# Optimization experiments

Hardware: AMD Instinct MI355X
Metric: run time of the kernel (lower is better)

The kernel has to match this reference:

```python
import jax, jax.numpy as jnp
import numpy as np

B, T, D = 2, 2048, 1024
F_DIM = 4096
E = 8


def setup_inputs() -> dict:
    key = jax.random.key(0)
    ks = jax.random.split(key, 6)
    x = jax.random.normal(ks[0], (B, T, D), dtype=jnp.float32)
    Wr = jax.random.normal(ks[1], (E, D), dtype=jnp.float32) * 0.02  # router weight [E, D]
    W1 = jax.random.normal(ks[2], (E, F_DIM, D), dtype=jnp.float32) * 0.02  # per-expert Linear(D->F) weights
    b1 = jnp.zeros((E, F_DIM), dtype=jnp.float32)
    W2 = jax.random.normal(ks[3], (E, D, F_DIM), dtype=jnp.float32) * 0.02  # per-expert Linear(F->D) weights
    b2 = jnp.zeros((E, D), dtype=jnp.float32)
    return {"x": x, "Wr": Wr, "W1": W1, "b1": b1, "W2": W2, "b2": b2, "top_k": 2}


def reference(x, Wr, W1, b1, W2, b2, top_k):
    # router scores: [b, t, E]
    scores = jnp.einsum('btd,ed->bte', x, Wr)
    topk_vals, topk_idx = jax.lax.top_k(scores, top_k)  # [b, t, k]
    # Dense compute over all experts (E is small); grouped-GEMM equivalent of the
    # original per-token loop. hidden: [b, t, E, F]
    h = jax.nn.relu(jnp.einsum('btd,efd->btef', x, W1) + b1)
    all_out = jnp.einsum('btef,edf->bted', h, W2) + b2  # [b, t, E, D]
    # gather the top-k experts' outputs per token: [b, t, k, D]
    gathered = jnp.take_along_axis(all_out, topk_idx[..., None], axis=2)
    # FAITHFUL to source: softmax over the sequence dim (dim=-1 of [b, t]),
    # applied independently per top-k slot.
    weight = jax.nn.softmax(topk_vals, axis=1)  # [b, t, k]
    out = jnp.sum(weight[..., None] * gathered, axis=2)  # [b, t, D]
    return out
```

## Files before the change

### kernel.cpp

```cpp
#include <hip/hip_runtime.h>
#include <stdint.h>

typedef short bf16x8 __attribute__((ext_vector_type(8)));
typedef float f32x4 __attribute__((ext_vector_type(4)));

#define NTOK 4096
#define DDIM 1024
#define FDIM 4096
#define NEXP 8
#define SEQ  2048

#define FB_MAXROWS 8704
#define FB_MAXTILES 136
#define G_MAXROWS 10240
#define G_MT 40

#define GLOAD16(g, l) __builtin_amdgcn_global_load_lds( \
    (const __attribute__((address_space(1))) unsigned int*)(const void*)(g), \
    (__attribute__((address_space(3))) unsigned int*)(l), 16, 0, 0)

#define SCHEDB() __builtin_amdgcn_sched_barrier(0)

__device__ __forceinline__ unsigned short f2bf(float f) {
    union { float f; unsigned int u; } v; v.f = f;
    unsigned int u = v.u;
    unsigned int r = (u + 0x7FFFu + ((u >> 16) & 1u)) >> 16;
    return (unsigned short)r;
}
__device__ __forceinline__ unsigned int pk2(float a, float b) {
    return (unsigned int)f2bf(a) | ((unsigned int)f2bf(b) << 16);
}

__global__ __launch_bounds__(256) void cvt_kernel(
    const float* __restrict__ src, unsigned short* __restrict__ dst, int n4)
{
    int i = blockIdx.x * 256 + threadIdx.x;
    const int stride = gridDim.x * 256;
    for (; i < n4; i += stride) {
        const float4 v = ((const float4*)src)[i];
        ushort4 o;
        o.x = f2bf(v.x); o.y = f2bf(v.y); o.z = f2bf(v.z); o.w = f2bf(v.w);
        ((ushort4*)dst)[i] = o;
    }
}

__global__ __launch_bounds__(256) void router_kernel(
    const float* __restrict__ x, const float* __restrict__ Wr,
    float* __restrict__ topk_vals, int* __restrict__ topk_idx,
    int* __restrict__ counts)
{
    const int wave = threadIdx.x >> 6;
    const int lane = threadIdx.x & 63;
    const int t = blockIdx.x * 4 + wave;
    const float4* xr = (const float4*)(x + (size_t)t * DDIM);

    float acc[NEXP];
#pragma unroll
    for (int e = 0; e < NEXP; ++e) acc[e] = 0.0f;

    for (int d = lane; d < DDIM / 4; d += 64) {
        const float4 xv = xr[d];
#pragma unroll
        for (int e = 0; e < NEXP; ++e) {
            const float4 wv = ((const float4*)(Wr + e * DDIM))[d];
            acc[e] = fmaf(xv.x, wv.x, acc[e]);
            acc[e] = fmaf(xv.y, wv.y, acc[e]);
            acc[e] = fmaf(xv.z, wv.z, acc[e]);
            acc[e] = fmaf(xv.w, wv.w, acc[e]);
        }
    }
#pragma unroll
    for (int e = 0; e < NEXP; ++e) {
        for (int off = 32; off > 0; off >>= 1)
            acc[e] += __shfl_xor(acc[e], off, 64);
    }
    if (lane == 0) {
        float best = -3.4e38f, second = -3.4e38f;
        int bi = 0, si = 0;
#pragma unroll
        for (int e = 0; e < NEXP; ++e) {
            const float s = acc[e];
            if (s > best) { second = best; si = bi; best = s; bi = e; }
            else if (s > second) { second = s; si = e; }
        }
        topk_vals[t * 2 + 0] = best;
        topk_vals[t * 2 + 1] = second;
        topk_idx[t * 2 + 0] = bi;
        topk_idx[t * 2 + 1] = si;
        atomicAdd(&counts[bi], 1);
        atomicAdd(&counts[si], 1);
    }
}

__global__ __launch_bounds__(256) void softmax_seq_kernel(
    const float* __restrict__ tv, float* __restrict__ weight)
{
    const int b = blockIdx.x >> 1;
    const int k = blockIdx.x & 1;
    const float* base = tv + (size_t)b * SEQ * 2 + k;
    float* wbase = weight + (size_t)b * SEQ * 2 + k;
    __shared__ float red[256];
    const int tid = threadIdx.x;

    float m = -3.4e38f;
    for (int t = tid; t < SEQ; t += 256) m = fmaxf(m, base[t * 2]);
    red[tid] = m; __syncthreads();
    for (int s = 128; s > 0; s >>= 1) {
        if (tid < s) red[tid] = fmaxf(red[tid], red[tid + s]);
        __syncthreads();
    }
    m = red[0];
    __syncthreads();

    float sum = 0.0f;
    for (int t = tid; t < SEQ; t += 256) sum += expf(base[t * 2] - m);
    red[tid] = sum; __syncthreads();
    for (int s = 128; s > 0; s >>= 1) {
        if (tid < s) red[tid] += red[tid + s];
        __syncthreads();
    }
    const float inv = 1.0f / red[0];
    for (int t = tid; t < SEQ; t += 256)
        wbase[t * 2] = expf(base[t * 2] - m) * inv;
}

__global__ void scan_kernel(const int* __restrict__ counts,
                            int* __restrict__ padOff, int* __restrict__ cursor,
                            int padBits)
{
    if (threadIdx.x == 0) {
        const int pad = (1 << padBits) - 1;
        int o = 0;
        for (int e = 0; e < NEXP; ++e) {
            padOff[e] = o;
            o += ((counts[e] + pad) >> padBits) << padBits;
        }
        padOff[NEXP] = o;
    }
    if (threadIdx.x < NEXP) cursor[threadIdx.x] = 0;
}

__global__ __launch_bounds__(256) void scatter_kernel(
    const int* __restrict__ topk_idx, const int* __restrict__ padOff,
    int* __restrict__ cursor, int* __restrict__ perm)
{
    const int t = blockIdx.x * 256 + threadIdx.x;
#pragma unroll
    for (int k = 0; k < 2; ++k) {
        const int e = topk_idx[t * 2 + k];
        const int pos = padOff[e] + atomicAdd(&cursor[e], 1);
        perm[pos] = t * 2 + k;
    }
}


__global__ __launch_bounds__(512, 2) void gemm1_g(
    const unsigned short* __restrict__ Xb, const unsigned short* __restrict__ Wb,
    const float* __restrict__ b1, const int* __restrict__ perm,
    const int* __restrict__ padOff, unsigned short* __restrict__ h)
{
    const int bid = blockIdx.x;
    const int swz = (bid & 7) * 80 + (bid >> 3);
    const int by = swz % G_MT;
    const int bx = swz / G_MT;
    const int row0 = by * 256;
    if (row0 >= padOff[NEXP]) return;
    int e = 0;
#pragma unroll
    for (int i = 1; i < NEXP; ++i) if (row0 >= padOff[i]) e = i;

    __shared__ unsigned short As[2][256 * 64];
    __shared__ unsigned short Bs[2][256 * 64];

    const int tid = threadIdx.x;
    const int w = tid >> 6, lane = tid & 63;
    const int wr = (w >> 2) * 128;
    const int wc = (w & 3) * 64;
    const int fr = lane & 15, kg = lane >> 4;
    const int col0 = bx * 256;

    const int gchunk = ((tid & 7) ^ ((tid >> 3) & 7)) * 8;
    const int lbase = (tid >> 3) * 64 + (tid & 7) * 8;

    const unsigned short* aSrc[4];
    const unsigned short* bSrc[4];
#pragma unroll
    for (int j = 0; j < 4; ++j) {
        const int r = j * 64 + (tid >> 3);
        const int pm = perm[row0 + r];
        const int tok = (pm >= 0) ? (pm >> 1) : 0;
        aSrc[j] = Xb + (size_t)tok * DDIM + gchunk;
        bSrc[j] = Wb + ((size_t)e * FDIM + col0 + r) * DDIM + gchunk;
    }

    f32x4 acc[8][4] = {};

#define STG1(buf, koff) do { \
    _Pragma("unroll") \
    for (int j = 0; j < 4; ++j) { \
        GLOAD16(aSrc[j] + (koff), &As[buf][j * 4096 + lbase]); \
        GLOAD16(bSrc[j] + (koff), &Bs[buf][j * 4096 + lbase]); \
    } } while (0)

    const int NT = DDIM / 64;
    STG1(0, 0);
    __syncthreads();

    int cur = 0;
    for (int t = 0; t < NT; ++t) {
        if (t + 1 < NT) STG1(cur ^ 1, (t + 1) * 64);
        SCHEDB();
        const unsigned short* Ab = &As[cur][0];
        const unsigned short* Bb = &Bs[cur][0];
#pragma unroll
        for (int kk = 0; kk < 2; ++kk) {
            bf16x8 a[8], b[4];
            const int cx = (((kk << 2) | kg)) ;
#pragma unroll
            for (int m = 0; m < 8; ++m)
                a[m] = *(const bf16x8*)&Ab[(wr + m * 16 + fr) * 64 + ((cx ^ (fr & 7)) << 3)];
#pragma unroll
            for (int n = 0; n < 4; ++n)
                b[n] = *(const bf16x8*)&Bb[(wc + n * 16 + fr) * 64 + ((cx ^ (fr & 7)) << 3)];
#pragma unroll
            for (int m = 0; m < 8; ++m)
#pragma unroll
                for (int n = 0; n < 4; ++n)
                    acc[m][n] = __builtin_amdgcn_mfma_f32_16x16x32_bf16(a[m], b[n], acc[m][n], 0, 0, 0);
        }
        __syncthreads();
        cur ^= 1;
    }
#undef STG1

#pragma unroll
    for (int n = 0; n < 4; ++n) {
        const int colg = col0 + wc + n * 16 + fr;
        const float bias = b1[e * FDIM + colg];
#pragma unroll
        for (int m = 0; m < 8; ++m) {
#pragma unroll
            for (int r = 0; r < 4; ++r) {
                const int rowg = row0 + wr + m * 16 + kg * 4 + r;
                h[(size_t)rowg * FDIM + colg] = f2bf(fmaxf(acc[m][n][r] + bias, 0.0f));
            }
        }
    }
}

__global__ __launch_bounds__(512, 2) void gemm2_g(
    const unsigned short* __restrict__ h, const unsigned short* __restrict__ Wb,
    const float* __restrict__ b2, const int* __restrict__ perm,
    const int* __restrict__ padOff, const float* __restrict__ weight,
    float* __restrict__ out)
{
    const int bid = blockIdx.x;
    const int swz = (bid & 7) * 80 + (bid >> 3);
    const int by = swz % G_MT;
    const int rest = swz / G_MT;
    const int bx = rest & 3;
    const int kc = rest >> 2;
    const int row0 = by * 256;
    if (row0 >= padOff[NEXP]) return;
    int e = 0;
#pragma unroll
    for (int i = 1; i < NEXP; ++i) if (row0 >= padOff[i]) e = i;

    __shared__ unsigned short As[2][256 * 64];
    __shared__ unsigned short Bs[2][256 * 64];

    const int tid = threadIdx.x;
    const int w = tid >> 6, lane = tid & 63;
    const int wr = (w >> 2) * 128;
    const int wc = (w & 3) * 64;
    const int fr = lane & 15, kg = lane >> 4;
    const int col0 = bx * 256;
    const int kbase = kc * (FDIM / 4);

    const int gchunk = ((tid & 7) ^ ((tid >> 3) & 7)) * 8;
    const int lbase = (tid >> 3) * 64 + (tid & 7) * 8;

    const unsigned short* aSrc[4];
    const unsigned short* bSrc[4];
#pragma unroll
    for (int j = 0; j < 4; ++j) {
        const int r = j * 64 + (tid >> 3);
        aSrc[j] = h + (size_t)(row0 + r) * FDIM + kbase + gchunk;
        bSrc[j] = Wb + ((size_t)e * DDIM + col0 + r) * FDIM + kbase + gchunk;
    }

    f32x4 acc[8][4] = {};

#define STG2(buf, koff) do { \
    _Pragma("unroll") \
    for (int j = 0; j < 4; ++j) { \
        GLOAD16(aSrc[j] + (koff), &As[buf][j * 4096 + lbase]); \
        GLOAD16(bSrc[j] + (koff), &Bs[buf][j * 4096 + lbase]); \
    } } while (0)

    const int NT = (FDIM / 4) / 64;
    STG2(0, 0);
    __syncthreads();

    int cur = 0;
    for (int t = 0; t < NT; ++t) {
        if (t + 1 < NT) STG2(cur ^ 1, (t + 1) * 64);
        SCHEDB();
        const unsigned short* Ab = &As[cur][0];
        const unsigned short* Bb = &Bs[cur][0];
#pragma unroll
        for (int kk = 0; kk < 2; ++kk) {
            bf16x8 a[8], b[4];
            const int cx = (((kk << 2) | kg));
#pragma unroll
            for (int m = 0; m < 8; ++m)
                a[m] = *(const bf16x8*)&Ab[(wr + m * 16 + fr) * 64 + ((cx ^ (fr & 7)) << 3)];
#pragma unroll
            for (int n = 0; n < 4; ++n)
                b[n] = *(const bf16x8*)&Bb[(wc + n * 16 + fr) * 64 + ((cx ^ (fr & 7)) << 3)];
#pragma unroll
            for (int m = 0; m < 8; ++m)
#pragma unroll
                for (int n = 0; n < 4; ++n)
                    acc[m][n] = __builtin_amdgcn_mfma_f32_16x16x32_bf16(a[m], b[n], acc[m][n], 0, 0, 0);
        }
        __syncthreads();
        cur ^= 1;
    }
#undef STG2

#pragma unroll
    for (int n = 0; n < 4; ++n) {
        const int colg = col0 + wc + n * 16 + fr;
        const float bias = (kc == 0) ? b2[e * DDIM + colg] : 0.0f;
#pragma unroll
        for (int m = 0; m < 8; ++m) {
#pragma unroll
            for (int r = 0; r < 4; ++r) {
                const int rowg = row0 + wr + m * 16 + kg * 4 + r;
                const int pm = perm[rowg];
                if (pm >= 0) {
                    const float wgt = weight[pm];
                    atomicAdd(&out[(size_t)(pm >> 1) * DDIM + colg], (acc[m][n][r] + bias) * wgt);
                }
            }
        }
    }
}


__global__ __launch_bounds__(256) void gemm1_fb(
    const float* __restrict__ x, const float* __restrict__ W1,
    const float* __restrict__ b1, const int* __restrict__ perm,
    const int* __restrict__ padOff, unsigned short* __restrict__ h)
{
    const int row0 = blockIdx.y * 64;
    if (row0 >= padOff[NEXP]) return;
    int e = 0;
#pragma unroll
    for (int i = 1; i < NEXP; ++i) if (row0 >= padOff[i]) e = i;

    __shared__ unsigned short As[64][40];
    __shared__ unsigned short Bs[64][40];

    const int tid = threadIdx.x;
    const int srow = tid >> 2;
    const int skp = (tid & 3) << 3;

    const int pm = perm[row0 + srow];
    const float* aSrc = (pm >= 0) ? (x + (size_t)(pm >> 1) * DDIM + skp) : 0;
    const int fRow = blockIdx.x * 64 + srow;
    const float* bSrc = W1 + ((size_t)e * FDIM + fRow) * DDIM + skp;

    const int lane = tid & 63;
    const int wm = ((tid >> 7) & 1) * 32;
    const int wn = ((tid >> 6) & 1) * 32;
    const int fr = lane & 15;
    const int kg = lane >> 4;

    f32x4 acc[2][2] = {{{0,0,0,0},{0,0,0,0}},{{0,0,0,0},{0,0,0,0}}};

    for (int k0 = 0; k0 < DDIM; k0 += 32) {
        uint4 av = make_uint4(0, 0, 0, 0);
        if (aSrc) {
            const float4 lo = *(const float4*)(aSrc + k0);
            const float4 hi = *(const float4*)(aSrc + k0 + 4);
            av.x = pk2(lo.x, lo.y); av.y = pk2(lo.z, lo.w);
            av.z = pk2(hi.x, hi.y); av.w = pk2(hi.z, hi.w);
        }
        const float4 bl = *(const float4*)(bSrc + k0);
        const float4 bh = *(const float4*)(bSrc + k0 + 4);
        uint4 bv;
        bv.x = pk2(bl.x, bl.y); bv.y = pk2(bl.z, bl.w);
        bv.z = pk2(bh.x, bh.y); bv.w = pk2(bh.z, bh.w);

        __syncthreads();
        *(uint4*)&As[srow][skp] = av;
        *(uint4*)&Bs[srow][skp] = bv;
        __syncthreads();

        const bf16x8 a0 = *(const bf16x8*)&As[wm + 0  + fr][kg << 3];
        const bf16x8 a1 = *(const bf16x8*)&As[wm + 16 + fr][kg << 3];
        const bf16x8 b0 = *(const bf16x8*)&Bs[wn + 0  + fr][kg << 3];
        const bf16x8 b1v = *(const bf16x8*)&Bs[wn + 16 + fr][kg << 3];
        acc[0][0] = __builtin_amdgcn_mfma_f32_16x16x32_bf16(a0, b0,  acc[0][0], 0, 0, 0);
        acc[0][1] = __builtin_amdgcn_mfma_f32_16x16x32_bf16(a0, b1v, acc[0][1], 0, 0, 0);
        acc[1][0] = __builtin_amdgcn_mfma_f32_16x16x32_bf16(a1, b0,  acc[1][0], 0, 0, 0);
        acc[1][1] = __builtin_amdgcn_mfma_f32_16x16x32_bf16(a1, b1v, acc[1][1], 0, 0, 0);
    }

#pragma unroll
    for (int mi = 0; mi < 2; ++mi)
#pragma unroll
        for (int ni = 0; ni < 2; ++ni) {
            const int colg = blockIdx.x * 64 + wn + ni * 16 + fr;
            const float bias = b1[e * FDIM + colg];
#pragma unroll
            for (int r = 0; r < 4; ++r) {
                const int rowg = row0 + wm + mi * 16 + (kg << 2) + r;
                float v = acc[mi][ni][r] + bias;
                v = fmaxf(v, 0.0f);
                h[(size_t)rowg * FDIM + colg] = f2bf(v);
            }
        }
}

__global__ __launch_bounds__(256) void gemm2_fb(
    const unsigned short* __restrict__ h, const float* __restrict__ W2,
    const float* __restrict__ b2, const int* __restrict__ perm,
    const int* __restrict__ padOff, const float* __restrict__ weight,
    float* __restrict__ out)
{
    const int row0 = blockIdx.y * 64;
    if (row0 >= padOff[NEXP]) return;
    int e = 0;
#pragma unroll
    for (int i = 1; i < NEXP; ++i) if (row0 >= padOff[i]) e = i;

    __shared__ unsigned short As[64][40];
    __shared__ unsigned short Bs[64][40];

    const int tid = threadIdx.x;
    const int srow = tid >> 2;
    const int skp = (tid & 3) << 3;

    const unsigned short* aSrc = h + (size_t)(row0 + srow) * FDIM + skp;
    const int dRow = blockIdx.x * 64 + srow;
    const float* bSrc = W2 + ((size_t)e * DDIM + dRow) * FDIM + skp;

    const int lane = tid & 63;
    const int wm = ((tid >> 7) & 1) * 32;
    const int wn = ((tid >> 6) & 1) * 32;
    const int fr = lane & 15;
    const int kg = lane >> 4;

    f32x4 acc[2][2] = {{{0,0,0,0},{0,0,0,0}},{{0,0,0,0},{0,0,0,0}}};

    for (int k0 = 0; k0 < FDIM; k0 += 32) {
        const uint4 av = *(const uint4*)(aSrc + k0);
        const float4 bl = *(const float4*)(bSrc + k0);
        const float4 bh = *(const float4*)(bSrc + k0 + 4);
        uint4 bv;
        bv.x = pk2(bl.x, bl.y); bv.y = pk2(bl.z, bl.w);
        bv.z = pk2(bh.x, bh.y); bv.w = pk2(bh.z, bh.w);

        __syncthreads();
        *(uint4*)&As[srow][skp] = av;
        *(uint4*)&Bs[srow][skp] = bv;
        __syncthreads();

        const bf16x8 a0 = *(const bf16x8*)&As[wm + 0  + fr][kg << 3];
        const bf16x8 a1 = *(const bf16x8*)&As[wm + 16 + fr][kg << 3];
        const bf16x8 b0 = *(const bf16x8*)&Bs[wn + 0  + fr][kg << 3];
        const bf16x8 b1v = *(const bf16x8*)&Bs[wn + 16 + fr][kg << 3];
        acc[0][0] = __builtin_amdgcn_mfma_f32_16x16x32_bf16(a0, b0,  acc[0][0], 0, 0, 0);
        acc[0][1] = __builtin_amdgcn_mfma_f32_16x16x32_bf16(a0, b1v, acc[0][1], 0, 0, 0);
        acc[1][0] = __builtin_amdgcn_mfma_f32_16x16x32_bf16(a1, b0,  acc[1][0], 0, 0, 0);
        acc[1][1] = __builtin_amdgcn_mfma_f32_16x16x32_bf16(a1, b1v, acc[1][1], 0, 0, 0);
    }

#pragma unroll
    for (int mi = 0; mi < 2; ++mi)
#pragma unroll
        for (int ni = 0; ni < 2; ++ni) {
            const int colg = blockIdx.x * 64 + wn + ni * 16 + fr;
            const float bias = b2[e * DDIM + colg];
#pragma unroll
            for (int r = 0; r < 4; ++r) {
                const int rowg = row0 + wm + mi * 16 + (kg << 2) + r;
                const int pm = perm[rowg];
                if (pm >= 0) {
                    const float w = weight[pm];
                    const float v = (acc[mi][ni][r] + bias) * w;
                    atomicAdd(&out[(size_t)(pm >> 1) * DDIM + colg], v);
                }
            }
        }
}

extern "C" void kernel_launch(void* const* d_in, const int* in_sizes, int n_in,
                              void* d_out, int out_size, void* d_ws, size_t ws_size,
                              hipStream_t stream)
{
    const float* x  = (const float*)d_in[0];
    const float* Wr = (const float*)d_in[1];
    const float* W1 = (const float*)d_in[2];
    const float* b1 = (const float*)d_in[3];
    const float* W2 = (const float*)d_in[4];
    const float* b2 = (const float*)d_in[5];
    float* out = (float*)d_out;
    char* ws = (char*)d_ws;

    float* topk_vals = (float*)(ws);
    float* weight    = (float*)(ws + 32768);
    int*   topk_idx  = (int*)(ws + 65536);
    int*   counts    = (int*)(ws + 98304);
    int*   padOff    = (int*)(ws + 98368);
    int*   cursor    = (int*)(ws + 98432);
    int*   perm      = (int*)(ws + 98496);

    const size_t NEED = 151257088ULL;

    if (ws_size >= NEED) {
        unsigned short* Xb = (unsigned short*)(ws + 262144);
        unsigned short* h  = (unsigned short*)(ws + 8650752);
        unsigned short* Wb = (unsigned short*)(ws + 92536832);

        hipMemsetAsync(counts, 0, NEXP * sizeof(int), stream);
        hipMemsetAsync(perm, 0xFF, G_MAXROWS * sizeof(int), stream);
        hipMemsetAsync(out, 0, (size_t)out_size * sizeof(float), stream);

        cvt_kernel<<<2048, 256, 0, stream>>>(x, Xb, NTOK * DDIM / 4);
        cvt_kernel<<<2048, 256, 0, stream>>>(W1, Wb, NEXP * FDIM * DDIM / 4);
        router_kernel<<<NTOK / 4, 256, 0, stream>>>(x, Wr, topk_vals, topk_idx, counts);
        softmax_seq_kernel<<<4, 256, 0, stream>>>(topk_vals, weight);
        scan_kernel<<<1, 64, 0, stream>>>(counts, padOff, cursor, 8);
        scatter_kernel<<<NTOK / 256, 256, 0, stream>>>(topk_idx, padOff, cursor, perm);

        gemm1_g<<<16 * G_MT, 512, 0, stream>>>(Xb, Wb, b1, perm, padOff, h);
        cvt_kernel<<<2048, 256, 0, stream>>>(W2, Wb, NEXP * DDIM * FDIM / 4);
        gemm2_g<<<16 * G_MT, 512, 0, stream>>>(h, Wb, b2, perm, padOff, weight, out);
    } else {
        unsigned short* h = (unsigned short*)(ws + 135168);

        hipMemsetAsync(counts, 0, NEXP * sizeof(int), stream);
        hipMemsetAsync(perm, 0xFF, FB_MAXROWS * sizeof(int), stream);
        hipMemsetAsync(out, 0, (size_t)out_size * sizeof(float), stream);

        router_kernel<<<NTOK / 4, 256, 0, stream>>>(x, Wr, topk_vals, topk_idx, counts);
        softmax_seq_kernel<<<4, 256, 0, stream>>>(topk_vals, weight);
        scan_kernel<<<1, 64, 0, stream>>>(counts, padOff, cursor, 6);
        scatter_kernel<<<NTOK / 256, 256, 0, stream>>>(topk_idx, padOff, cursor, perm);

        gemm1_fb<<<dim3(FDIM / 64, FB_MAXTILES), 256, 0, stream>>>(x, W1, b1, perm, padOff, h);
        gemm2_fb<<<dim3(DDIM / 64, FB_MAXTILES), 256, 0, stream>>>(h, W2, b2, perm, padOff, weight, out);
    }
}
```

Baseline: 609.0 us.

## Use BK=32 two-stage-ahead LDS pipeline with manual waitcnt and halve GEMM2 split-K

Measured after the change: 612.9 us. No clear change (+0.6%).

```diff
diff --git a/kernel.cpp b/kernel.cpp
--- a/kernel.cpp
+++ b/kernel.cpp
@@ -19,7 +19,11 @@
     (const __attribute__((address_space(1))) unsigned int*)(const void*)(g), \
     (__attribute__((address_space(3))) unsigned int*)(l), 16, 0, 0)
 
-#define SCHEDB() __builtin_amdgcn_sched_barrier(0)
+#define WAIT_LGKM0() asm volatile("s_waitcnt lgkmcnt(0)" ::: "memory")
+#define WAIT_VM4()   asm volatile("s_waitcnt vmcnt(4)" ::: "memory")
+#define WAIT_VM0()   asm volatile("s_waitcnt vmcnt(0)" ::: "memory")
+#define SBAR()       __builtin_amdgcn_s_barrier()
+#define SCHEDB()     __builtin_amdgcn_sched_barrier(0)
 
 __device__ __forceinline__ unsigned short f2bf(float f) {
     union { float f; unsigned int u; } v; v.f = f;
@@ -169,8 +173,8 @@
 #pragma unroll
     for (int i = 1; i < NEXP; ++i) if (row0 >= padOff[i]) e = i;
 
-    __shared__ unsigned short As[2][256 * 64];
-    __shared__ unsigned short Bs[2][256 * 64];
+    __shared__ unsigned short As[2][256 * 32];
+    __shared__ unsigned short Bs[2][256 * 32];
 
     const int tid = threadIdx.x;
     const int w = tid >> 6, lane = tid & 63;
@@ -179,57 +183,53 @@
     const int fr = lane & 15, kg = lane >> 4;
     const int col0 = bx * 256;
 
-    const int gchunk = ((tid & 7) ^ ((tid >> 3) & 7)) * 8;
-    const int lbase = (tid >> 3) * 64 + (tid & 7) * 8;
-
-    const unsigned short* aSrc[4];
-    const unsigned short* bSrc[4];
-#pragma unroll
-    for (int j = 0; j < 4; ++j) {
-        const int r = j * 64 + (tid >> 3);
+    const int srow = tid >> 2;
+    const int gch = ((tid & 3) ^ (srow & 3)) * 8;
+    const unsigned short* aS[2];
+    const unsigned short* bS[2];
+#pragma unroll
+    for (int j = 0; j < 2; ++j) {
+        const int r = j * 128 + srow;
         const int pm = perm[row0 + r];
         const int tok = (pm >= 0) ? (pm >> 1) : 0;
-        aSrc[j] = Xb + (size_t)tok * DDIM + gchunk;
-        bSrc[j] = Wb + ((size_t)e * FDIM + col0 + r) * DDIM + gchunk;
+        aS[j] = Xb + (size_t)tok * DDIM + gch;
+        bS[j] = Wb + ((size_t)e * FDIM + col0 + r) * DDIM + gch;
     }
 
     f32x4 acc[8][4] = {};
 
-#define STG1(buf, koff) do { \
-    _Pragma("unroll") \
-    for (int j = 0; j < 4; ++j) { \
-        GLOAD16(aSrc[j] + (koff), &As[buf][j * 4096 + lbase]); \
-        GLOAD16(bSrc[j] + (koff), &Bs[buf][j * 4096 + lbase]); \
+#define STG1(buf, koff) do { _Pragma("unroll") \
+    for (int j = 0; j < 2; ++j) { \
+        GLOAD16(aS[j] + (koff), &As[buf][(j * 512 + tid) * 8]); \
+        GLOAD16(bS[j] + (koff), &Bs[buf][(j * 512 + tid) * 8]); \
     } } while (0)
 
-    const int NT = DDIM / 64;
+    const int NT = DDIM / 32;
     STG1(0, 0);
-    __syncthreads();
-
-    int cur = 0;
+    STG1(1, 32);
+    SCHEDB(); WAIT_VM4(); SBAR(); SCHEDB();
+
     for (int t = 0; t < NT; ++t) {
-        if (t + 1 < NT) STG1(cur ^ 1, (t + 1) * 64);
+        const int cur = t & 1;
+        bf16x8 a[8], b[4];
+        const int rch = (kg ^ (fr & 3)) << 3;
+#pragma unroll
+        for (int m = 0; m < 8; ++m)
+            a[m] = *(const bf16x8*)&As[cur][(wr + m * 16 + fr) * 32 + rch];
+#pragma unroll
+        for (int n = 0; n < 4; ++n)
+            b[n] = *(const bf16x8*)&Bs[cur][(wc + n * 16 + fr) * 32 + rch];
+        WAIT_LGKM0(); SCHEDB();
+        SBAR(); SCHEDB();
+        if (t + 2 < NT) STG1(cur, (t + 2) * 32);
+#pragma unroll
+        for (int m = 0; m < 8; ++m)
+#pragma unroll
+            for (int n = 0; n < 4; ++n)
+                acc[m][n] = __builtin_amdgcn_mfma_f32_16x16x32_bf16(a[m], b[n], acc[m][n], 0, 0, 0);
         SCHEDB();
-        const unsigned short* Ab = &As[cur][0];
-        const unsigned short* Bb = &Bs[cur][0];
-#pragma unroll
-        for (int kk = 0; kk < 2; ++kk) {
-            bf16x8 a[8], b[4];
-            const int cx = (((kk << 2) | kg)) ;
-#pragma unroll
-            for (int m = 0; m < 8; ++m)
-                a[m] = *(const bf16x8*)&Ab[(wr + m * 16 + fr) * 64 + ((cx ^ (fr & 7)) << 3)];
-#pragma unroll
-            for (int n = 0; n < 4; ++n)
-                b[n] = *(const bf16x8*)&Bb[(wc + n * 16 + fr) * 64 + ((cx ^ (fr & 7)) << 3)];
-#pragma unroll
-            for (int m = 0; m < 8; ++m)
-#pragma unroll
-                for (int n = 0; n < 4; ++n)
-                    acc[m][n] = __builtin_amdgcn_mfma_f32_16x16x32_bf16(a[m], b[n], acc[m][n], 0, 0, 0);
-        }
-        __syncthreads();
-        cur ^= 1;
+        if (t + 2 < NT) { WAIT_VM4(); } else { WAIT_VM0(); }
+        SBAR(); SCHEDB();
     }
 #undef STG1
 
@@ -255,7 +255,7 @@
     float* __restrict__ out)
 {
     const int bid = blockIdx.x;
-    const int swz = (bid & 7) * 80 + (bid >> 3);
+    const int swz = (bid & 7) * 40 + (bid >> 3);
     const int by = swz % G_MT;
     const int rest = swz / G_MT;
     const int bx = rest & 3;
@@ -266,8 +266,8 @@
 #pragma unroll
     for (int i = 1; i < NEXP; ++i) if (row0 >= padOff[i]) e = i;
 
-    __shared__ unsigned short As[2][256 * 64];
-    __shared__ unsigned short Bs[2][256 * 64];
+    __shared__ unsigned short As[2][256 * 32];
+    __shared__ unsigned short Bs[2][256 * 32];
 
     const int tid = threadIdx.x;
     const int w = tid >> 6, lane = tid & 63;
@@ -275,57 +275,53 @@
     const int wc = (w & 3) * 64;
     const int fr = lane & 15, kg = lane >> 4;
     const int col0 = bx * 256;
-    const int kbase = kc * (FDIM / 4);
-
-    const int gchunk = ((tid & 7) ^ ((tid >> 3) & 7)) * 8;
-    const int lbase = (tid >> 3) * 64 + (tid & 7) * 8;
-
-    const unsigned short* aSrc[4];
-    const unsigned short* bSrc[4];
-#pragma unroll
-    for (int j = 0; j < 4; ++j) {
-        const int r = j * 64 + (tid >> 3);
-        aSrc[j] = h + (size_t)(row0 + r) * FDIM + kbase + gchunk;
-        bSrc[j] = Wb + ((size_t)e * DDIM + col0 + r) * FDIM + kbase + gchunk;
+    const int kbase = kc * (FDIM / 2);
+
+    const int srow = tid >> 2;
+    const int gch = ((tid & 3) ^ (srow & 3)) * 8;
+    const unsigned short* aS[2];
+    const unsigned short* bS[2];
+#pragma unroll
+    for (int j = 0; j < 2; ++j) {
+        const int r = j * 128 + srow;
+        aS[j] = h + (size_t)(row0 + r) * FDIM + kbase + gch;
+        bS[j] = Wb + ((size_t)e * DDIM + col0 + r) * FDIM + kbase + gch;
     }
 
     f32x4 acc[8][4] = {};
 
-#define STG2(buf, koff) do { \
-    _Pragma("unroll") \
-    for (int j = 0; j < 4; ++j) { \
-        GLOAD16(aSrc[j] + (koff), &As[buf][j * 4096 + lbase]); \
-        GLOAD16(bSrc[j] + (koff), &Bs[buf][j * 4096 + lbase]); \
+#define STG2(buf, koff) do { _Pragma("unroll") \
+    for (int j = 0; j < 2; ++j) { \
+        GLOAD16(aS[j] + (koff), &As[buf][(j * 512 + tid) * 8]); \
+        GLOAD16(bS[j] + (koff), &Bs[buf][(j * 512 + tid) * 8]); \
     } } while (0)
 
-    const int NT = (FDIM / 4) / 64;
+    const int NT = (FDIM / 2) / 32;
     STG2(0, 0);
-    __syncthreads();
-
-    int cur = 0;
+    STG2(1, 32);
+    SCHEDB(); WAIT_VM4(); SBAR(); SCHEDB();
+
     for (int t = 0; t < NT; ++t) {
-        if (t + 1 < NT) STG2(cur ^ 1, (t + 1) * 64);
+        const int cur = t & 1;
+        bf16x8 a[8], b[4];
+        const int rch = (kg ^ (fr & 3)) << 3;
+#pragma unroll
+        for (int m = 0; m < 8; ++m)
+            a[m] = *(const bf16x8*)&As[cur][(wr + m * 16 + fr) * 32 + rch];
+#pragma unroll
+        for (int n = 0; n < 4; ++n)
+            b[n] = *(const bf16x8*)&Bs[cur][(wc + n * 16 + fr) * 32 + rch];
+        WAIT_LGKM0(); SCHEDB();
+        SBAR(); SCHEDB();
+        if (t + 2 < NT) STG2(cur, (t + 2) * 32);
+#pragma unroll
+        for (int m = 0; m < 8; ++m)
+#pragma unroll
+            for (int n = 0; n < 4; ++n)
+                acc[m][n] = __builtin_amdgcn_mfma_f32_16x16x32_bf16(a[m], b[n], acc[m][n], 0, 0, 0);
         SCHEDB();
-        const unsigned short* Ab = &As[cur][0];
-        const unsigned short* Bb = &Bs[cur][0];
-#pragma unroll
-        for (int kk = 0; kk < 2; ++kk) {
-            bf16x8 a[8], b[4];
-            const int cx = (((kk << 2) | kg));
-#pragma unroll
-            for (int m = 0; m < 8; ++m)
-                a[m] = *(const bf16x8*)&Ab[(wr + m * 16 + fr) * 64 + ((cx ^ (fr & 7)) << 3)];
-#pragma unroll
-            for (int n = 0; n < 4; ++n)
-                b[n] = *(const bf16x8*)&Bb[(wc + n * 16 + fr) * 64 + ((cx ^ (fr & 7)) << 3)];
-#pragma unroll
-            for (int m = 0; m < 8; ++m)
-#pragma unroll
-                for (int n = 0; n < 4; ++n)
-                    acc[m][n] = __builtin_amdgcn_mfma_f32_16x16x32_bf16(a[m], b[n], acc[m][n], 0, 0, 0);
-        }
-        __syncthreads();
-        cur ^= 1;
+        if (t + 2 < NT) { WAIT_VM4(); } else { WAIT_VM0(); }
+        SBAR(); SCHEDB();
     }
 #undef STG2
 
@@ -519,7 +515,7 @@
     int*   cursor    = (int*)(ws + 98432);
     int*   perm      = (int*)(ws + 98496);
 
-    const size_t NEED = 151257088ULL;
+    const size_t NEED = 159645696ULL;
 
     if (ws_size >= NEED) {
         unsigned short* Xb = (unsigned short*)(ws + 262144);
@@ -539,9 +535,9 @@
 
         gemm1_g<<<16 * G_MT, 512, 0, stream>>>(Xb, Wb, b1, perm, padOff, h);
         cvt_kernel<<<2048, 256, 0, stream>>>(W2, Wb, NEXP * DDIM * FDIM / 4);
-        gemm2_g<<<16 * G_MT, 512, 0, stream>>>(h, Wb, b2, perm, padOff, weight, out);
+        gemm2_g<<<8 * G_MT, 512, 0, stream>>>(h, Wb, b2, perm, padOff, weight, out);
     } else {
-        unsigned short* h = (unsigned short*)(ws + 135168);
+        unsigned short* h = (unsigned short*)(ws + 172032);
 
         hipMemsetAsync(counts, 0, NEXP * sizeof(int), stream);
         hipMemsetAsync(perm, 0xFF, FB_MAXROWS * sizeof(int), stream);
```
